# Performance work log

Measured on AMD Instinct MI355X. Metric: run time of the kernel, lower is better.

The kernel has to match this reference:

```python
import jax, jax.numpy as jnp
import numpy as np

N, E, B = 50000, 800000, 512
D_IN = 128
H = [128, 128, 128, 256, 128]
OUT = 2


def setup_inputs() -> dict:
    key = jax.random.key(0)
    ks = jax.random.split(key, 24)

    def w(k, i, o):
        return (jax.random.normal(k, (i, o), jnp.float32) / np.sqrt(i)).astype(jnp.float32)

    x = jax.random.normal(ks[0], (N, D_IN), jnp.float32)
    edge_index = jax.random.randint(ks[1], (2, E), 0, N)
    batch = (jnp.arange(N) * B) // N  # sorted graph ids, every graph non-empty

    return {
        "x": x,
        "edge_index": edge_index,
        "batch": batch,
        # SAGEConv k: out = mean_aggr(x_j) @ Wl + bl + x @ Wr  (PyG default: bias on lin_l, none on lin_r)
        "Wl1": w(ks[2], D_IN, H[0]), "Wr1": w(ks[3], D_IN, H[0]), "bl1": jnp.zeros((H[0],), jnp.float32),
        "Wl2": w(ks[4], H[0], H[1]), "Wr2": w(ks[5], H[0], H[1]), "bl2": jnp.zeros((H[1],), jnp.float32),
        "Wl3": w(ks[6], H[1], H[2]), "Wr3": w(ks[7], H[1], H[2]), "bl3": jnp.zeros((H[2],), jnp.float32),
        "W_f1": w(ks[8], H[2], H[3]), "b_f1": jnp.zeros((H[3],), jnp.float32),
        "W_f2": w(ks[9], H[3], H[4]), "b_f2": jnp.zeros((H[4],), jnp.float32),
        "W_sm": w(ks[10], H[4], OUT), "b_sm": jnp.zeros((OUT,), jnp.float32),
        "W_news": w(ks[11], D_IN, OUT), "b_news": jnp.zeros((OUT,), jnp.float32),
        "W_cat": w(ks[12], 2 * OUT, 1), "b_cat": jnp.zeros((1,), jnp.float32),
    }


def _sage(x, src, dst, Wl, Wr, bl):
    # mean aggregation of source-node features onto destination nodes
    msg = x[src]                                                     # [E, d] gather
    s = jax.ops.segment_sum(msg, dst, num_segments=N)                # [N, d] scatter-add
    cnt = jax.ops.segment_sum(jnp.ones((src.shape[0],), x.dtype), dst, num_segments=N)
    mean = s / jnp.maximum(cnt, 1.0)[:, None]
    return mean @ Wl + bl + x @ Wr


def reference(x, edge_index, batch, Wl1, Wr1, bl1, Wl2, Wr2, bl2, Wl3, Wr3, bl3,
              W_f1, b_f1, W_f2, b_f2, W_sm, b_sm, W_news, b_news, W_cat, b_cat):
    src, dst = edge_index[0], edge_index[1]
    h = jax.nn.relu(_sage(x, src, dst, Wl1, Wr1, bl1))
    h = jax.nn.relu(_sage(h, src, dst, Wl2, Wr2, bl2))
    h = jax.nn.relu(_sage(h, src, dst, Wl3, Wr3, bl3))

    h = jax.ops.segment_max(h, batch, num_segments=B)                # global_max_pool -> [B, H2]
    h = jax.nn.relu(h @ W_f1 + b_f1)
    h = jax.nn.relu(h @ W_f2 + b_f2)
    h = jax.nn.relu(h @ W_sm + b_sm)                                 # [B, OUT]

    # root = first node index of each graph (batch is sorted)
    root = jax.ops.segment_min(jnp.arange(N), batch, num_segments=B)  # [B]
    news = jax.nn.relu(x[root] @ W_news + b_news)                    # [B, OUT]

    out = jnp.concatenate([h, news], axis=-1) @ W_cat + b_cat        # [B, 1]
    return jax.nn.sigmoid(out)
```

## Files before the change

kernel.cpp:

```cpp
#include <hip/hip_runtime.h>
#include <hip/hip_bf16.h>
#include <math.h>

#define D 128
#define SA 144

typedef __attribute__((ext_vector_type(8))) short bf16x8;
typedef __attribute__((ext_vector_type(4))) float f32x4;

static __device__ __forceinline__ short f2b(float f) {
    unsigned u = __builtin_bit_cast(unsigned, f);
    unsigned r = (u + 0x7FFFu + ((u >> 16) & 1u)) >> 16;
    return (short)r;
}
static __device__ __forceinline__ float b2f(short b) {
    unsigned u = ((unsigned)(unsigned short)b) << 16;
    return __builtin_bit_cast(float, u);
}


struct PrepArgs {
    const float* x; short* xb; int total4; int xb_blocks;
    const float* w[6]; short* wo[6]; int w_blocks;
    const int* dst; int* bcnt; int E;
};

__global__ __launch_bounds__(256) void prep_kernel(PrepArgs a) {
    int bid = blockIdx.x, tid = threadIdx.x;
    if (bid < a.xb_blocks) {
        int idx = bid * 256 + tid;
        if (idx < a.total4) {
            float4 v = ((const float4*)a.x)[idx];
            short4 o;
            o.x = f2b(v.x); o.y = f2b(v.y); o.z = f2b(v.z); o.w = f2b(v.w);
            ((short4*)a.xb)[idx] = o;
        }
        return;
    }
    if (bid < a.xb_blocks + a.w_blocks) {
        int idx4 = (bid - a.xb_blocks) * 256 + tid;
        int base = idx4 * 4;
        int m = base >> 14;
        int i = base & 16383;
        const float* W = a.w[m];
        short* O = a.wo[m];
        int k = i >> 7, nn = i & 127;
        float4 v = *(const float4*)(W + k * D + nn);
        O[(nn + 0) * D + k] = f2b(v.x);
        O[(nn + 1) * D + k] = f2b(v.y);
        O[(nn + 2) * D + k] = f2b(v.z);
        O[(nn + 3) * D + k] = f2b(v.w);
        return;
    }
    __shared__ int hist[512];
    hist[tid] = 0; hist[tid + 256] = 0;
    __syncthreads();
    int e0 = (bid - a.xb_blocks - a.w_blocks) * 4096;
#pragma unroll
    for (int i = 0; i < 16; ++i) {
        int e = e0 + i * 256 + tid;
        if (e < a.E) atomicAdd(&hist[a.dst[e] >> 7], 1);
    }
    __syncthreads();
    int c = hist[tid];       if (c) atomicAdd(&a.bcnt[tid], c);
    c = hist[tid + 256];     if (c) atomicAdd(&a.bcnt[tid + 256], c);
}


__global__ __launch_bounds__(256) void scan512_kernel(const int* __restrict__ bcnt,
                                                      int* __restrict__ gbase,
                                                      int* __restrict__ gcursor) {
    __shared__ int sc[256];
    int tid = threadIdx.x;
    int a0 = bcnt[2 * tid], a1 = bcnt[2 * tid + 1];
    int s = a0 + a1;
    sc[tid] = s;
    __syncthreads();
    for (int off = 1; off < 256; off <<= 1) {
        int t = (tid >= off) ? sc[tid - off] : 0;
        __syncthreads();
        sc[tid] += t;
        __syncthreads();
    }
    int ex = sc[tid] - s;
    gbase[2 * tid] = ex;         gcursor[2 * tid] = ex;
    gbase[2 * tid + 1] = ex + a0; gcursor[2 * tid + 1] = ex + a0;
    if (tid == 255) gbase[512] = sc[255];
}


#define EPB 4096
__global__ __launch_bounds__(256) void bin_kernel(const int* __restrict__ src,
                                                  const int* __restrict__ dst,
                                                  int* __restrict__ gcursor,
                                                  int2* __restrict__ binned, int E) {
    __shared__ int hist[512];
    __shared__ int base[512];
    int tid = threadIdx.x;
    int e0 = blockIdx.x * EPB;
    hist[tid] = 0; hist[tid + 256] = 0;
    __syncthreads();
    int sv[16], dv[16], bv[16];
#pragma unroll
    for (int i = 0; i < 16; ++i) {
        int e = e0 + i * 256 + tid;
        if (e < E) {
            sv[i] = src[e]; dv[i] = dst[e];
            bv[i] = dv[i] >> 7;
            atomicAdd(&hist[bv[i]], 1);
        } else bv[i] = -1;
    }
    __syncthreads();
    {
        int c0 = hist[tid];
        base[tid] = c0 ? atomicAdd(&gcursor[tid], c0) : 0;
        hist[tid] = 0;
        int c1 = hist[tid + 256];
        base[tid + 256] = c1 ? atomicAdd(&gcursor[tid + 256], c1) : 0;
        hist[tid + 256] = 0;
    }
    __syncthreads();
#pragma unroll
    for (int i = 0; i < 16; ++i) {
        if (bv[i] >= 0) {
            int off = atomicAdd(&hist[bv[i]], 1);
            binned[base[bv[i]] + off] = make_int2(sv[i], dv[i]);
        }
    }
}


__global__ __launch_bounds__(256) void place_kernel(const int2* __restrict__ binned,
                                                    const int* __restrict__ gbase,
                                                    int* __restrict__ row_ptr,
                                                    float* __restrict__ inv_deg,
                                                    int* __restrict__ col,
                                                    int n, int E, int NB) {
    __shared__ int cnt[128];
    __shared__ int sc[128];
    __shared__ int cur[128];
    int b = blockIdx.x, tid = threadIdx.x;
    int node0 = b << 7;
    int node1 = node0 + 128; if (node1 > n) node1 = n;
    int start = gbase[b], end = gbase[b + 1];
    if (tid < 128) cnt[tid] = 0;
    __syncthreads();
    for (int i = start + tid; i < end; i += 256)
        atomicAdd(&cnt[binned[i].y & 127], 1);
    __syncthreads();
    if (tid < 128) sc[tid] = cnt[tid];
    __syncthreads();
    for (int off = 1; off < 128; off <<= 1) {
        int t = (tid < 128 && tid >= off) ? sc[tid - off] : 0;
        __syncthreads();
        if (tid < 128) sc[tid] += t;
        __syncthreads();
    }
    if (tid < 128) {
        int nd = node0 + tid;
        if (nd < node1) {
            int c = cnt[tid];
            int base = start + sc[tid] - c;
            row_ptr[nd] = base;
            inv_deg[nd] = 1.0f / (float)((c > 0) ? c : 1);
            cur[tid] = base;
        }
    }
    if (b == NB - 1 && tid == 0) row_ptr[n] = E;
    __syncthreads();
    for (int i = start + tid; i < end; i += 256) {
        int2 e = binned[i];
        int pos = atomicAdd(&cur[e.y & 127], 1);
        col[pos] = e.x;
    }
}


__global__ void agg_kernel(const short* __restrict__ h, const int* __restrict__ row_ptr,
                           const int* __restrict__ col, const float* __restrict__ inv_deg,
                           short* __restrict__ out, int n) {
    int w = (blockIdx.x * blockDim.x + threadIdx.x) >> 6;
    int lane = threadIdx.x & 63;
    if (w >= n) return;
    int s = row_ptr[w], e = row_ptr[w + 1];
    int g = lane >> 4, l16 = lane & 15;
    float acc[8];
#pragma unroll
    for (int q = 0; q < 8; ++q) acc[q] = 0.f;
    int p = s + g;
    for (; p + 4 < e; p += 8) {
        int j0 = col[p];
        int j1 = col[p + 4];
        bf16x8 v0 = *(const bf16x8*)(h + (size_t)j0 * D + l16 * 8);
        bf16x8 v1 = *(const bf16x8*)(h + (size_t)j1 * D + l16 * 8);
#pragma unroll
        for (int q = 0; q < 8; ++q) acc[q] += b2f(v0[q]);
#pragma unroll
        for (int q = 0; q < 8; ++q) acc[q] += b2f(v1[q]);
    }
    if (p < e) {
        int j = col[p];
        bf16x8 v = *(const bf16x8*)(h + (size_t)j * D + l16 * 8);
#pragma unroll
        for (int q = 0; q < 8; ++q) acc[q] += b2f(v[q]);
    }
#pragma unroll
    for (int q = 0; q < 8; ++q) {
        acc[q] += __shfl_xor(acc[q], 16, 64);
        acc[q] += __shfl_xor(acc[q], 32, 64);
    }
    if (g == 0) {
        float sc = inv_deg[w];
        bf16x8 o;
#pragma unroll
        for (int q = 0; q < 8; ++q) o[q] = f2b(acc[q] * sc);
        *(bf16x8*)(out + (size_t)w * D + l16 * 8) = o;
    }
}


__global__ __launch_bounds__(256) void sage_mm_mfma(
        const short* __restrict__ Aagg, const short* __restrict__ Hin,
        const short* __restrict__ WlT,  const short* __restrict__ WrT,
        const float* __restrict__ bl,   short* __restrict__ out, int M) {
    __shared__ short lA[128 * SA];
    __shared__ short lW[128 * SA];
    int tid  = threadIdx.x;
    int wave = tid >> 6, lane = tid & 63;
    int row0 = blockIdx.x * 128;
    int mrow = wave * 32;
    int m16  = lane & 15, quad = lane >> 4;

    f32x4 acc[2][8];
#pragma unroll
    for (int i = 0; i < 2; ++i)
#pragma unroll
        for (int j = 0; j < 8; ++j) acc[i][j] = (f32x4){0.f, 0.f, 0.f, 0.f};

#pragma unroll
    for (int half = 0; half < 2; ++half) {
        const short* A = half ? Hin : Aagg;
        const short* W = half ? WrT : WlT;
#pragma unroll
        for (int it = 0; it < 8; ++it) {
            int idx = it * 256 + tid;
            int r = idx >> 4, c8 = (idx & 15) << 3;
            bf16x8 va = {0, 0, 0, 0, 0, 0, 0, 0};
            int gr = row0 + r;
            if (gr < M) va = *(const bf16x8*)(A + (size_t)gr * D + c8);
            *(bf16x8*)(&lA[r * SA + c8]) = va;
            bf16x8 vw = *(const bf16x8*)(W + r * D + c8);
            *(bf16x8*)(&lW[r * SA + c8]) = vw;
        }
        __syncthreads();
#pragma unroll
        for (int ks = 0; ks < 4; ++ks) {
            int kb = ks * 32 + quad * 8;
            bf16x8 a0 = *(const bf16x8*)(&lA[(mrow +      m16) * SA + kb]);
            bf16x8 a1 = *(const bf16x8*)(&lA[(mrow + 16 + m16) * SA + kb]);
#pragma unroll
            for (int nt = 0; nt < 8; ++nt) {
                bf16x8 b = *(const bf16x8*)(&lW[(nt * 16 + m16) * SA + kb]);
                acc[0][nt] = __builtin_amdgcn_mfma_f32_16x16x32_bf16(a0, b, acc[0][nt], 0, 0, 0);
                acc[1][nt] = __builtin_amdgcn_mfma_f32_16x16x32_bf16(a1, b, acc[1][nt], 0, 0, 0);
            }
        }
        __syncthreads();
    }
#pragma unroll
    for (int mt = 0; mt < 2; ++mt) {
#pragma unroll
        for (int r = 0; r < 4; ++r) {
            int grow = row0 + mrow + mt * 16 + quad * 4 + r;
            if (grow < M) {
#pragma unroll
                for (int nt = 0; nt < 8; ++nt) {
                    int gcol = nt * 16 + m16;
                    float v = acc[mt][nt][r] + bl[gcol];
                    out[(size_t)grow * D + gcol] = f2b(fmaxf(v, 0.f));
                }
            }
        }
    }
}


__global__ __launch_bounds__(256) void poolhead_kernel(
        const short* __restrict__ h, const int* __restrict__ batch,
        const float* __restrict__ x,
        const float* __restrict__ W_f1, const float* __restrict__ b_f1,
        const float* __restrict__ W_f2, const float* __restrict__ b_f2,
        const float* __restrict__ W_sm, const float* __restrict__ b_sm,
        const float* __restrict__ W_news, const float* __restrict__ b_news,
        const float* __restrict__ W_cat, const float* __restrict__ b_cat,
        float* __restrict__ out, int n) {
    int g = blockIdx.x;
    int tid = threadIdx.x;
    int f = tid & 127, half = tid >> 7;
    __shared__ float pm[256];
    __shared__ float p[128], t1[256], t2[128], hs[2], nw[2];
    int lo = 0, hi = n;
    while (lo < hi) { int m = (lo + hi) >> 1; if (batch[m] < g) lo = m + 1; else hi = m; }
    int start = lo;
    hi = n;
    while (lo < hi) { int m = (lo + hi) >> 1; if (batch[m] < g + 1) lo = m + 1; else hi = m; }
    int end = lo;
    float m = -3.4e38f;
    for (int i = start + half; i < end; i += 2) m = fmaxf(m, b2f(h[(size_t)i * D + f]));
    pm[tid] = m;
    __syncthreads();
    if (tid < 128) p[tid] = fmaxf(pm[tid], pm[tid + 128]);
    __syncthreads();
    float a1 = b_f1[tid];
    for (int k = 0; k < 128; ++k) a1 += p[k] * W_f1[k * 256 + tid];
    t1[tid] = fmaxf(a1, 0.f);
    __syncthreads();
    if (tid < 128) {
        float a2 = b_f2[tid];
        for (int k = 0; k < 256; ++k) a2 += t1[k] * W_f2[k * 128 + tid];
        t2[tid] = fmaxf(a2, 0.f);
    }
    __syncthreads();
    if (tid < 2) {
        float a3 = b_sm[tid];
        for (int k = 0; k < 128; ++k) a3 += t2[k] * W_sm[k * 2 + tid];
        hs[tid] = fmaxf(a3, 0.f);
        const float* xr = x + (size_t)start * D;
        float a4 = b_news[tid];
        for (int k = 0; k < 128; ++k) a4 += xr[k] * W_news[k * 2 + tid];
        nw[tid] = fmaxf(a4, 0.f);
    }
    __syncthreads();
    if (tid == 0) {
        float o = b_cat[0] + hs[0] * W_cat[0] + hs[1] * W_cat[1]
                           + nw[0] * W_cat[2] + nw[1] * W_cat[3];
        out[g] = 1.0f / (1.0f + __expf(-o));
    }
}


extern "C" void kernel_launch(void* const* d_in, const int* in_sizes, int n_in,
                              void* d_out, int out_size, void* d_ws, size_t ws_size,
                              hipStream_t stream) {
    const float* x      = (const float*)d_in[0];
    const int*   edge   = (const int*)d_in[1];
    const int*   batch  = (const int*)d_in[2];
    const float* Wl1 = (const float*)d_in[3];
    const float* Wr1 = (const float*)d_in[4];
    const float* bl1 = (const float*)d_in[5];
    const float* Wl2 = (const float*)d_in[6];
    const float* Wr2 = (const float*)d_in[7];
    const float* bl2 = (const float*)d_in[8];
    const float* Wl3 = (const float*)d_in[9];
    const float* Wr3 = (const float*)d_in[10];
    const float* bl3 = (const float*)d_in[11];
    const float* W_f1 = (const float*)d_in[12];
    const float* b_f1 = (const float*)d_in[13];
    const float* W_f2 = (const float*)d_in[14];
    const float* b_f2 = (const float*)d_in[15];
    const float* W_sm = (const float*)d_in[16];
    const float* b_sm = (const float*)d_in[17];
    const float* W_news = (const float*)d_in[18];
    const float* b_news = (const float*)d_in[19];
    const float* W_cat = (const float*)d_in[20];
    const float* b_cat = (const float*)d_in[21];
    float* out = (float*)d_out;

    const int E = in_sizes[1] / 2;
    const int n = in_sizes[2];
    const int B = out_size;

    const int* src = edge;
    const int* dst = edge + E;

    char* ws = (char*)d_ws;
    size_t off = 0;
    auto carve = [&](size_t bytes) {
        void* pt = ws + off;
        off = (off + bytes + 255) & ~(size_t)255;
        return pt;
    };
    int*   row_ptr = (int*)carve((size_t)(n + 1) * 4);
    float* inv_deg = (float*)carve((size_t)n * 4);
    int*   col     = (int*)carve((size_t)E * 4);
    int*   bcnt    = (int*)carve((size_t)512 * 4);
    int*   gbase   = (int*)carve((size_t)513 * 4);
    int*   gcursor = (int*)carve((size_t)512 * 4);
    int2*  binned  = (int2*)carve((size_t)E * 8);
    short* xb      = (short*)carve((size_t)n * D * 2);
    short* aggb    = (short*)carve((size_t)n * D * 2);
    short* hA      = (short*)carve((size_t)n * D * 2);
    short* hB      = (short*)carve((size_t)n * D * 2);
    short* Wt[6];
    for (int i = 0; i < 6; ++i) Wt[i] = (short*)carve((size_t)D * D * 2);
    (void)ws_size;

    hipMemsetAsync(bcnt, 0, 512 * 4, stream);
    PrepArgs pa;
    pa.x = x; pa.xb = xb; pa.total4 = n * D / 4;
    pa.xb_blocks = (pa.total4 + 255) / 256;
    pa.w[0] = Wl1; pa.w[1] = Wr1; pa.w[2] = Wl2; pa.w[3] = Wr2; pa.w[4] = Wl3; pa.w[5] = Wr3;
    for (int i = 0; i < 6; ++i) pa.wo[i] = Wt[i];
    pa.w_blocks = (6 * D * D) / 1024;
    pa.dst = dst; pa.bcnt = bcnt; pa.E = E;
    int h_blocks = (E + 4095) / 4096;
    prep_kernel<<<pa.xb_blocks + pa.w_blocks + h_blocks, 256, 0, stream>>>(pa);

    int NB = (n + 127) / 128;
    scan512_kernel<<<1, 256, 0, stream>>>(bcnt, gbase, gcursor);
    bin_kernel<<<(E + EPB - 1) / EPB, 256, 0, stream>>>(src, dst, gcursor, binned, E);
    place_kernel<<<NB, 256, 0, stream>>>(binned, gbase, row_ptr, inv_deg, col, n, E, NB);

    int agg_blocks = (n * 64 + 255) / 256;
    int mm_blocks  = (n + 127) / 128;

    agg_kernel<<<agg_blocks, 256, 0, stream>>>(xb, row_ptr, col, inv_deg, aggb, n);
    sage_mm_mfma<<<mm_blocks, 256, 0, stream>>>(aggb, xb, Wt[0], Wt[1], bl1, hA, n);
    agg_kernel<<<agg_blocks, 256, 0, stream>>>(hA, row_ptr, col, inv_deg, aggb, n);
    sage_mm_mfma<<<mm_blocks, 256, 0, stream>>>(aggb, hA, Wt[2], Wt[3], bl2, hB, n);
    agg_kernel<<<agg_blocks, 256, 0, stream>>>(hB, row_ptr, col, inv_deg, aggb, n);
    sage_mm_mfma<<<mm_blocks, 256, 0, stream>>>(aggb, hB, Wt[4], Wt[5], bl3, hA, n);

    poolhead_kernel<<<B, 256, 0, stream>>>(hA, batch, x,
                                           W_f1, b_f1, W_f2, b_f2, W_sm, b_sm,
                                           W_news, b_news, W_cat, b_cat, out, n);
}
```

Before: 316.2 us.

## Fuse neighbor aggregation into SAGE matmul kernel and pack binned edges

Merges the separate aggregation and MFMA matmul kernels into one per-layer kernel. Each block aggregates neighbor means for its 128 nodes straight into shared memory and then runs both matmuls, reading the weight fragments directly from global memory instead of staging them in LDS. This removes the aggregated-feature round trip through global memory and three kernel launches. Binned edges are also packed into 32-bit words (source index plus low destination bits), which halves the binning traffic. The trade-off is that only 391 blocks each process 32 nodes per wave serially, which lowers gather parallelism and may hurt latency hiding.

```diff
diff --git a/kernel.cpp b/kernel.cpp
--- a/kernel.cpp
+++ b/kernel.cpp
@@ -83,7 +83,7 @@
         __syncthreads();
     }
     int ex = sc[tid] - s;
-    gbase[2 * tid] = ex;         gcursor[2 * tid] = ex;
+    gbase[2 * tid] = ex;          gcursor[2 * tid] = ex;
     gbase[2 * tid + 1] = ex + a0; gcursor[2 * tid + 1] = ex + a0;
     if (tid == 255) gbase[512] = sc[255];
 }
@@ -93,20 +93,21 @@
 __global__ __launch_bounds__(256) void bin_kernel(const int* __restrict__ src,
                                                   const int* __restrict__ dst,
                                                   int* __restrict__ gcursor,
-                                                  int2* __restrict__ binned, int E) {
+                                                  unsigned* __restrict__ binned, int E) {
     __shared__ int hist[512];
     __shared__ int base[512];
     int tid = threadIdx.x;
     int e0 = blockIdx.x * EPB;
     hist[tid] = 0; hist[tid + 256] = 0;
     __syncthreads();
-    int sv[16], dv[16], bv[16];
+    unsigned pk[16]; int bv[16];
 #pragma unroll
     for (int i = 0; i < 16; ++i) {
         int e = e0 + i * 256 + tid;
         if (e < E) {
-            sv[i] = src[e]; dv[i] = dst[e];
-            bv[i] = dv[i] >> 7;
+            int s = src[e], d = dst[e];
+            bv[i] = d >> 7;
+            pk[i] = (unsigned)s | ((unsigned)(d & 127) << 25);
             atomicAdd(&hist[bv[i]], 1);
         } else bv[i] = -1;
     }
@@ -124,13 +125,13 @@
     for (int i = 0; i < 16; ++i) {
         if (bv[i] >= 0) {
             int off = atomicAdd(&hist[bv[i]], 1);
-            binned[base[bv[i]] + off] = make_int2(sv[i], dv[i]);
-        }
-    }
-}
-
-
-__global__ __launch_bounds__(256) void place_kernel(const int2* __restrict__ binned,
+            binned[base[bv[i]] + off] = pk[i];
+        }
+    }
+}
+
+
+__global__ __launch_bounds__(256) void place_kernel(const unsigned* __restrict__ binned,
                                                     const int* __restrict__ gbase,
                                                     int* __restrict__ row_ptr,
                                                     float* __restrict__ inv_deg,
@@ -146,7 +147,7 @@
     if (tid < 128) cnt[tid] = 0;
     __syncthreads();
     for (int i = start + tid; i < end; i += 256)
-        atomicAdd(&cnt[binned[i].y & 127], 1);
+        atomicAdd(&cnt[binned[i] >> 25], 1);
     __syncthreads();
     if (tid < 128) sc[tid] = cnt[tid];
     __syncthreads();
@@ -169,68 +170,68 @@
     if (b == NB - 1 && tid == 0) row_ptr[n] = E;
     __syncthreads();
     for (int i = start + tid; i < end; i += 256) {
-        int2 e = binned[i];
-        int pos = atomicAdd(&cur[e.y & 127], 1);
-        col[pos] = e.x;
-    }
-}
-
-
-__global__ void agg_kernel(const short* __restrict__ h, const int* __restrict__ row_ptr,
-                           const int* __restrict__ col, const float* __restrict__ inv_deg,
-                           short* __restrict__ out, int n) {
-    int w = (blockIdx.x * blockDim.x + threadIdx.x) >> 6;
-    int lane = threadIdx.x & 63;
-    if (w >= n) return;
-    int s = row_ptr[w], e = row_ptr[w + 1];
-    int g = lane >> 4, l16 = lane & 15;
-    float acc[8];
-#pragma unroll
-    for (int q = 0; q < 8; ++q) acc[q] = 0.f;
-    int p = s + g;
-    for (; p + 4 < e; p += 8) {
-        int j0 = col[p];
-        int j1 = col[p + 4];
-        bf16x8 v0 = *(const bf16x8*)(h + (size_t)j0 * D + l16 * 8);
-        bf16x8 v1 = *(const bf16x8*)(h + (size_t)j1 * D + l16 * 8);
-#pragma unroll
-        for (int q = 0; q < 8; ++q) acc[q] += b2f(v0[q]);
-#pragma unroll
-        for (int q = 0; q < 8; ++q) acc[q] += b2f(v1[q]);
-    }
-    if (p < e) {
-        int j = col[p];
-        bf16x8 v = *(const bf16x8*)(h + (size_t)j * D + l16 * 8);
-#pragma unroll
-        for (int q = 0; q < 8; ++q) acc[q] += b2f(v[q]);
-    }
-#pragma unroll
-    for (int q = 0; q < 8; ++q) {
-        acc[q] += __shfl_xor(acc[q], 16, 64);
-        acc[q] += __shfl_xor(acc[q], 32, 64);
-    }
-    if (g == 0) {
-        float sc = inv_deg[w];
-        bf16x8 o;
-#pragma unroll
-        for (int q = 0; q < 8; ++q) o[q] = f2b(acc[q] * sc);
-        *(bf16x8*)(out + (size_t)w * D + l16 * 8) = o;
-    }
-}
-
-
-__global__ __launch_bounds__(256) void sage_mm_mfma(
-        const short* __restrict__ Aagg, const short* __restrict__ Hin,
+        unsigned e = binned[i];
+        int pos = atomicAdd(&cur[e >> 25], 1);
+        col[pos] = (int)(e & 0x01FFFFFFu);
+    }
+}
+
+
+__global__ __launch_bounds__(256, 4) void sage_layer_kernel(
+        const short* __restrict__ Hin,
+        const int* __restrict__ row_ptr, const int* __restrict__ col,
+        const float* __restrict__ inv_deg,
         const short* __restrict__ WlT,  const short* __restrict__ WrT,
         const float* __restrict__ bl,   short* __restrict__ out, int M) {
     __shared__ short lA[128 * SA];
-    __shared__ short lW[128 * SA];
     int tid  = threadIdx.x;
     int wave = tid >> 6, lane = tid & 63;
     int row0 = blockIdx.x * 128;
+    int g = lane >> 4, l16 = lane & 15;
+
+    for (int t = 0; t < 32; ++t) {
+        int lrow = wave * 32 + t;
+        int node = row0 + lrow;
+        float acc[8];
+#pragma unroll
+        for (int q = 0; q < 8; ++q) acc[q] = 0.f;
+        if (node < M) {
+            int s = row_ptr[node], e = row_ptr[node + 1];
+            int p = s + g;
+            for (; p + 4 < e; p += 8) {
+                int j0 = col[p];
+                int j1 = col[p + 4];
+                bf16x8 v0 = *(const bf16x8*)(Hin + (size_t)j0 * D + l16 * 8);
+                bf16x8 v1 = *(const bf16x8*)(Hin + (size_t)j1 * D + l16 * 8);
+#pragma unroll
+                for (int q = 0; q < 8; ++q) acc[q] += b2f(v0[q]);
+#pragma unroll
+                for (int q = 0; q < 8; ++q) acc[q] += b2f(v1[q]);
+            }
+            if (p < e) {
+                int j = col[p];
+                bf16x8 v = *(const bf16x8*)(Hin + (size_t)j * D + l16 * 8);
+#pragma unroll
+                for (int q = 0; q < 8; ++q) acc[q] += b2f(v[q]);
+            }
+        }
+#pragma unroll
+        for (int q = 0; q < 8; ++q) {
+            acc[q] += __shfl_xor(acc[q], 16, 64);
+            acc[q] += __shfl_xor(acc[q], 32, 64);
+        }
+        if (g == 0) {
+            float sc = (node < M) ? inv_deg[node] : 0.f;
+            bf16x8 o;
+#pragma unroll
+            for (int q = 0; q < 8; ++q) o[q] = f2b(acc[q] * sc);
+            *(bf16x8*)(&lA[lrow * SA + l16 * 8]) = o;
+        }
+    }
+    __syncthreads();
+
     int mrow = wave * 32;
-    int m16  = lane & 15, quad = lane >> 4;
-
+    int m16 = l16, quad = lane >> 4;
     f32x4 acc[2][8];
 #pragma unroll
     for (int i = 0; i < 2; ++i)
@@ -238,34 +239,39 @@
         for (int j = 0; j < 8; ++j) acc[i][j] = (f32x4){0.f, 0.f, 0.f, 0.f};
 
 #pragma unroll
-    for (int half = 0; half < 2; ++half) {
-        const short* A = half ? Hin : Aagg;
-        const short* W = half ? WrT : WlT;
-#pragma unroll
-        for (int it = 0; it < 8; ++it) {
-            int idx = it * 256 + tid;
-            int r = idx >> 4, c8 = (idx & 15) << 3;
-            bf16x8 va = {0, 0, 0, 0, 0, 0, 0, 0};
-            int gr = row0 + r;
-            if (gr < M) va = *(const bf16x8*)(A + (size_t)gr * D + c8);
-            *(bf16x8*)(&lA[r * SA + c8]) = va;
-            bf16x8 vw = *(const bf16x8*)(W + r * D + c8);
-            *(bf16x8*)(&lW[r * SA + c8]) = vw;
-        }
-        __syncthreads();
-#pragma unroll
-        for (int ks = 0; ks < 4; ++ks) {
-            int kb = ks * 32 + quad * 8;
-            bf16x8 a0 = *(const bf16x8*)(&lA[(mrow +      m16) * SA + kb]);
-            bf16x8 a1 = *(const bf16x8*)(&lA[(mrow + 16 + m16) * SA + kb]);
-#pragma unroll
-            for (int nt = 0; nt < 8; ++nt) {
-                bf16x8 b = *(const bf16x8*)(&lW[(nt * 16 + m16) * SA + kb]);
-                acc[0][nt] = __builtin_amdgcn_mfma_f32_16x16x32_bf16(a0, b, acc[0][nt], 0, 0, 0);
-                acc[1][nt] = __builtin_amdgcn_mfma_f32_16x16x32_bf16(a1, b, acc[1][nt], 0, 0, 0);
-            }
-        }
-        __syncthreads();
+    for (int ks = 0; ks < 4; ++ks) {
+        int kb = ks * 32 + quad * 8;
+        bf16x8 a0 = *(const bf16x8*)(&lA[(mrow +      m16) * SA + kb]);
+        bf16x8 a1 = *(const bf16x8*)(&lA[(mrow + 16 + m16) * SA + kb]);
+#pragma unroll
+        for (int nt = 0; nt < 8; ++nt) {
+            bf16x8 b = *(const bf16x8*)(WlT + (nt * 16 + m16) * D + kb);
+            acc[0][nt] = __builtin_amdgcn_mfma_f32_16x16x32_bf16(a0, b, acc[0][nt], 0, 0, 0);
+            acc[1][nt] = __builtin_amdgcn_mfma_f32_16x16x32_bf16(a1, b, acc[1][nt], 0, 0, 0);
+        }
+    }
+    __syncthreads();
+#pragma unroll
+    for (int it = 0; it < 8; ++it) {
+        int idx = it * 256 + tid;
+        int r = idx >> 4, c8 = (idx & 15) << 3;
+        bf16x8 va = {0, 0, 0, 0, 0, 0, 0, 0};
+        int gr = row0 + r;
+        if (gr < M) va = *(const bf16x8*)(Hin + (size_t)gr * D + c8);
+        *(bf16x8*)(&lA[r * SA + c8]) = va;
+    }
+    __syncthreads();
+#pragma unroll
+    for (int ks = 0; ks < 4; ++ks) {
+        int kb = ks * 32 + quad * 8;
+        bf16x8 a0 = *(const bf16x8*)(&lA[(mrow +      m16) * SA + kb]);
+        bf16x8 a1 = *(const bf16x8*)(&lA[(mrow + 16 + m16) * SA + kb]);
+#pragma unroll
+        for (int nt = 0; nt < 8; ++nt) {
+            bf16x8 b = *(const bf16x8*)(WrT + (nt * 16 + m16) * D + kb);
+            acc[0][nt] = __builtin_amdgcn_mfma_f32_16x16x32_bf16(a0, b, acc[0][nt], 0, 0, 0);
+            acc[1][nt] = __builtin_amdgcn_mfma_f32_16x16x32_bf16(a1, b, acc[1][nt], 0, 0, 0);
+        }
     }
 #pragma unroll
     for (int mt = 0; mt < 2; ++mt) {
@@ -380,17 +386,16 @@
         off = (off + bytes + 255) & ~(size_t)255;
         return pt;
     };
-    int*   row_ptr = (int*)carve((size_t)(n + 1) * 4);
-    float* inv_deg = (float*)carve((size_t)n * 4);
-    int*   col     = (int*)carve((size_t)E * 4);
-    int*   bcnt    = (int*)carve((size_t)512 * 4);
-    int*   gbase   = (int*)carve((size_t)513 * 4);
-    int*   gcursor = (int*)carve((size_t)512 * 4);
-    int2*  binned  = (int2*)carve((size_t)E * 8);
-    short* xb      = (short*)carve((size_t)n * D * 2);
-    short* aggb    = (short*)carve((size_t)n * D * 2);
-    short* hA      = (short*)carve((size_t)n * D * 2);
-    short* hB      = (short*)carve((size_t)n * D * 2);
+    int*      row_ptr = (int*)carve((size_t)(n + 1) * 4);
+    float*    inv_deg = (float*)carve((size_t)n * 4);
+    int*      col     = (int*)carve((size_t)E * 4);
+    int*      bcnt    = (int*)carve((size_t)512 * 4);
+    int*      gbase   = (int*)carve((size_t)513 * 4);
+    int*      gcursor = (int*)carve((size_t)512 * 4);
+    unsigned* binned  = (unsigned*)carve((size_t)E * 4);
+    short*    xb      = (short*)carve((size_t)n * D * 2);
+    short*    hA      = (short*)carve((size_t)n * D * 2);
+    short*    hB      = (short*)carve((size_t)n * D * 2);
     short* Wt[6];
     for (int i = 0; i < 6; ++i) Wt[i] = (short*)carve((size_t)D * D * 2);
     (void)ws_size;
@@ -411,15 +416,12 @@
     bin_kernel<<<(E + EPB - 1) / EPB, 256, 0, stream>>>(src, dst, gcursor, binned, E);
     place_kernel<<<NB, 256, 0, stream>>>(binned, gbase, row_ptr, inv_deg, col, n, E, NB);
 
-    int agg_blocks = (n * 64 + 255) / 256;
-    int mm_blocks  = (n + 127) / 128;
-
-    agg_kernel<<<agg_blocks, 256, 0, stream>>>(xb, row_ptr, col, inv_deg, aggb, n);
-    sage_mm_mfma<<<mm_blocks, 256, 0, stream>>>(aggb, xb, Wt[0], Wt[1], bl1, hA, n);
-    agg_kernel<<<agg_blocks, 256, 0, stream>>>(hA, row_ptr, col, inv_deg, aggb, n);
-    sage_mm_mfma<<<mm_blocks, 256, 0, stream>>>(aggb, hA, Wt[2], Wt[3], bl2, hB, n);
-    agg_kernel<<<agg_blocks, 256, 0, stream>>>(hB, row_ptr, col, inv_deg, aggb, n);
-    sage_mm_mfma<<<mm_blocks, 256, 0, stream>>>(aggb, hB, Wt[4], Wt[5], bl3, hA, n);
+    sage_layer_kernel<<<NB, 256, 0, stream>>>(xb, row_ptr, col, inv_deg,
+                                              Wt[0], Wt[1], bl1, hA, n);
+    sage_layer_kernel<<<NB, 256, 0, stream>>>(hA, row_ptr, col, inv_deg,
+                                              Wt[2], Wt[3], bl2, hB, n);
+    sage_layer_kernel<<<NB, 256, 0, stream>>>(hB, row_ptr, col, inv_deg,
+                                              Wt[4], Wt[5], bl3, hA, n);
 
     poolhead_kernel<<<B, 256, 0, stream>>>(hA, batch, x,
                                            W_f1, b_f1, W_f2, b_f2, W_sm, b_sm,
```

Result: slower. 499.2 us (+57.9%).
